# Kernel optimization log

Hardware: AMD Instinct MI355X
Metric: run time of the kernel (lower is better)

## Reference

```python
import jax, jax.numpy as jnp
import numpy as np

N = 50000          # nodes
E_RAND = 800000    # random edges (avg degree 16)
D_IN = 128
H = 4              # heads (both layers)
C = 64             # per-head channels (both layers)
NEG_SLOPE = 0.2    # PyG GATConv default leaky_relu slope


def _gat_conv(x, src, dst, W, att_src, att_dst, bias, concat):
    """PyG GATConv (dropout=0, self-loops already in edge list).
    x:[N,Din] W:[Din,H*C] att_*:[H,C] bias:[H*C] or [C]."""
    n = x.shape[0]
    h = (x @ W).reshape(n, H, C)                      # [N,H,C]
    a_src = jnp.sum(h * att_src, axis=-1)             # [N,H]
    a_dst = jnp.sum(h * att_dst, axis=-1)             # [N,H]
    e = jax.nn.leaky_relu(a_src[src] + a_dst[dst], NEG_SLOPE)  # [E,H]
    # segment softmax over incoming edges of each destination node
    m = jax.ops.segment_max(e, dst, num_segments=n)    # [N,H]
    e = jnp.exp(e - m[dst])
    denom = jax.ops.segment_sum(e, dst, num_segments=n)
    alpha = e / (denom[dst] + 1e-16)                   # [E,H]
    msg = h[src] * alpha[..., None]                    # [E,H,C]
    out = jax.ops.segment_sum(msg, dst, num_segments=n)  # [N,H,C]
    if concat:
        out = out.reshape(n, H * C)
    else:
        out = out.mean(axis=1)
    return out + bias


def setup_inputs() -> dict:
    key = jax.random.key(0)
    ks = jax.random.split(key, 10)
    x = jax.random.normal(ks[0], (N, D_IN), jnp.float32)
    src = jax.random.randint(ks[1], (E_RAND,), 0, N)
    dst = jax.random.randint(ks[2], (E_RAND,), 0, N)
    loops = jnp.arange(N)  # add_self_loops=True (PyG default)
    edge_index = jnp.stack([jnp.concatenate([src, loops]),
                            jnp.concatenate([dst, loops])]).astype(jnp.int32)
    g = lambda k, shp, fan: (jax.random.normal(k, shp, jnp.float32) / np.float32(np.sqrt(fan)))
    W1 = g(ks[3], (D_IN, H * C), D_IN)
    att_src1 = g(ks[4], (H, C), C)
    att_dst1 = g(ks[5], (H, C), C)
    b1 = jnp.zeros((H * C,), jnp.float32)
    W2 = g(ks[6], (H * C, H * C), H * C)
    att_src2 = g(ks[7], (H, C), C)
    att_dst2 = g(ks[8], (H, C), C)
    b2 = jnp.zeros((C,), jnp.float32)
    return {"x": x, "edge_index": edge_index,
            "W1": W1, "att_src1": att_src1, "att_dst1": att_dst1, "b1": b1,
            "W2": W2, "att_src2": att_src2, "att_dst2": att_dst2, "b2": b2}


def reference(x, edge_index, W1, att_src1, att_dst1, b1, W2, att_src2, att_dst2, b2):
    src, dst = edge_index[0], edge_index[1]
    h = jax.nn.relu(_gat_conv(x, src, dst, W1, att_src1, att_dst1, b1, concat=True))
    h = jax.nn.relu(_gat_conv(h, src, dst, W2, att_src2, att_dst2, b2, concat=False))
    return jax.nn.softmax(h, axis=1)
```

## Files before the change

kernel.cpp:

```cpp
#include <hip/hip_runtime.h>


typedef __attribute__((ext_vector_type(8))) short short8;
typedef __attribute__((ext_vector_type(4))) float f32x4;
typedef __attribute__((ext_vector_type(2))) float f32x2;

static __device__ __forceinline__ ushort f2bf(float f) {
  uint u = __float_as_uint(f);
  return (ushort)((u + 0x7FFFu + ((u >> 16) & 1u)) >> 16);
}
static __device__ __forceinline__ float bf2f(ushort s) {
  return __uint_as_float(((uint)s) << 16);
}
static __device__ __forceinline__ unsigned char f2fp8(float f) {
  int p = __builtin_amdgcn_cvt_pk_fp8_f32(f, f, 0, false);
  return (unsigned char)(p & 0xFF);
}
static __device__ __forceinline__ uint4 cvt8bf(const float4& a, const float4& b) {
  uint4 hh;
  hh.x = (uint)f2bf(a.x) | ((uint)f2bf(a.y) << 16);
  hh.y = (uint)f2bf(a.z) | ((uint)f2bf(a.w) << 16);
  hh.z = (uint)f2bf(b.x) | ((uint)f2bf(b.y) << 16);
  hh.w = (uint)f2bf(b.z) | ((uint)f2bf(b.w) << 16);
  return hh;
}

__global__ __launch_bounds__(256)
void k_prep_hist(const float* __restrict__ W1, const float* __restrict__ W2,
                 ushort* __restrict__ w1th, ushort* __restrict__ w1tl,
                 ushort* __restrict__ w2th, ushort* __restrict__ w2tl,
                 const int* __restrict__ dstv, int* __restrict__ cnt,
                 int* __restrict__ pe, int E,
                 const float* __restrict__ x, ushort* __restrict__ xb,
                 int ng ) {
  const int b = blockIdx.x;
  const int eb = (E + 255) >> 8;
  if (b < 128) {
    int gid = b * 256 + threadIdx.x;
    int c = gid & 255, k = gid >> 8;
    float w = W1[(size_t)k * 256 + c];
    ushort h = f2bf(w);
    w1th[(size_t)c * 128 + k] = h;
    w1tl[(size_t)c * 128 + k] = f2bf(w - bf2f(h));
  } else if (b < 384) {
    int gid = (b - 128) * 256 + threadIdx.x;
    int c = gid & 255, k = gid >> 8;
    float w = W2[(size_t)k * 256 + c];
    ushort h = f2bf(w);
    w2th[(size_t)c * 256 + k] = h;
    w2tl[(size_t)c * 256 + k] = f2bf(w - bf2f(h));
  } else if (b < 384 + eb) {
    int i = (b - 384) * 256 + threadIdx.x;
    if (i < E) pe[i] = atomicAdd(&cnt[dstv[i]], 1);
  } else {
    int i = (b - 384 - eb) * 256 + threadIdx.x;
    if (i < ng) {
      const float4* xp = (const float4*)x + (size_t)i * 2;
      float4 a = xp[0], bb = xp[1];
      ((uint4*)xb)[i] = cvt8bf(a, bb);
    }
  }
}

__global__ __launch_bounds__(256)
void k_scan(const int* __restrict__ cnt, int* __restrict__ rowptr,
            int* __restrict__ bsum, int* __restrict__ bflag, int N, int E) {
  __shared__ int sm[256];
  __shared__ int s_prev;
  const int b = blockIdx.x, tid = threadIdx.x;
  const int gid = b * 256 + tid;
  int v = (gid < N) ? cnt[gid] : 0;
  sm[tid] = v;
  __syncthreads();
  for (int off = 1; off < 256; off <<= 1) {
    int t = (tid >= off) ? sm[tid - off] : 0;
    __syncthreads();
    sm[tid] += t;
    __syncthreads();
  }
  if (tid == 255) {
    atomicExch(&bsum[b], sm[255]);
    __threadfence();
    atomicExch(&bflag[b], 1);
  }
  if (tid == 0) s_prev = 0;
  __syncthreads();
  if (tid < b) {
    while (atomicAdd(&bflag[tid], 0) == 0) {}
    atomicAdd(&s_prev, atomicAdd(&bsum[tid], 0));
  }
  __syncthreads();
  if (gid < N) rowptr[gid] = s_prev + sm[tid] - v;
  if (gid == 0) rowptr[N] = E;
}

template <int K>
static __device__ __forceinline__
void gemm_body(int bid, const ushort* __restrict__ Ah,
               const ushort* __restrict__ Bth, const ushort* __restrict__ Btl,
               unsigned char* __restrict__ hout, int Nrows,
               const float* __restrict__ att_s, const float* __restrict__ att_d,
               float* __restrict__ a_s, float* __restrict__ a_d) {
  const int nrb = (Nrows + 127) >> 7;
  const int rb = (bid >> 4) * 8 + (bid & 7);
  const int ch = (bid >> 3) & 1;
  if (rb >= nrb) return;
  const int row0 = rb * 128;
  const int col0 = ch * 128;

  const int t = threadIdx.x;
  const int lane = t & 63;
  const int w = t >> 6;
  const int wr = (w >> 1) * 64;
  const int wc = (w & 1) * 64;

  const int fr = lane & 15;
  const int fq = lane >> 4;

  const ushort* arow[4];
#pragma unroll
  for (int r = 0; r < 4; r++) {
    int gr = row0 + wr + r * 16 + fr;
    gr = gr < Nrows ? gr : Nrows - 1;
    arow[r] = Ah + (size_t)gr * K + fq * 8;
  }
  const ushort* bb_h = Bth + (size_t)(col0 + wc + fr) * K + fq * 8;
  const ushort* bb_l = Btl + (size_t)(col0 + wc + fr) * K + fq * 8;

  f32x4 acc[4][4] = {};

#pragma unroll
  for (int k0 = 0; k0 < K; k0 += 32) {
    short8 fa[4], fbh[4], fbl[4];
#pragma unroll
    for (int r = 0; r < 4; r++)
      fa[r] = *(const short8*)(arow[r] + k0);
#pragma unroll
    for (int c = 0; c < 4; c++) {
      fbh[c] = *(const short8*)(bb_h + (size_t)c * 16 * K + k0);
      fbl[c] = *(const short8*)(bb_l + (size_t)c * 16 * K + k0);
    }
#pragma unroll
    for (int r = 0; r < 4; r++)
#pragma unroll
      for (int c = 0; c < 4; c++) {
        acc[r][c] = __builtin_amdgcn_mfma_f32_16x16x32_bf16(fa[r], fbh[c], acc[r][c], 0, 0, 0);
        acc[r][c] = __builtin_amdgcn_mfma_f32_16x16x32_bf16(fa[r], fbl[c], acc[r][c], 0, 0, 0);
      }
  }

#pragma unroll
  for (int r = 0; r < 4; r++)
#pragma unroll
    for (int c = 0; c < 4; c++) {
      int colg = col0 + wc + c * 16 + fr;
#pragma unroll
      for (int reg = 0; reg < 4; reg++) {
        int gr = row0 + wr + r * 16 + fq * 4 + reg;
        if (gr < Nrows)
          hout[(size_t)gr * 256 + colg] = f2fp8(acc[r][c][reg]);
      }
    }

  const int head = (col0 + wc) >> 6;
  float asv[4], adv[4];
#pragma unroll
  for (int c = 0; c < 4; c++) {
    asv[c] = att_s[col0 + wc + c * 16 + fr];
    adv[c] = att_d[col0 + wc + c * 16 + fr];
  }
#pragma unroll
  for (int r = 0; r < 4; r++)
#pragma unroll
    for (int reg = 0; reg < 4; reg++) {
      float ps = 0.f, pd = 0.f;
#pragma unroll
      for (int c = 0; c < 4; c++) {
        ps += acc[r][c][reg] * asv[c];
        pd += acc[r][c][reg] * adv[c];
      }
      ps += __shfl_xor(ps, 1); pd += __shfl_xor(pd, 1);
      ps += __shfl_xor(ps, 2); pd += __shfl_xor(pd, 2);
      ps += __shfl_xor(ps, 4); pd += __shfl_xor(pd, 4);
      ps += __shfl_xor(ps, 8); pd += __shfl_xor(pd, 8);
      if (fr == 0) {
        int gr = row0 + wr + r * 16 + fq * 4 + reg;
        if (gr < Nrows) {
          a_s[(size_t)gr * 4 + head] = ps;
          a_d[(size_t)gr * 4 + head] = pd;
        }
      }
    }
}

__global__ __launch_bounds__(256, 2)
void k_gemm1_scatter(const ushort* __restrict__ xb,
                     const ushort* __restrict__ Bth,
                     const ushort* __restrict__ Btl,
                     unsigned char* __restrict__ hout, int Nrows,
                     const float* __restrict__ att_s,
                     const float* __restrict__ att_d,
                     float* __restrict__ a_s, float* __restrict__ a_d,
                     const int* __restrict__ srcv, const int* __restrict__ dstv,
                     const int* __restrict__ rowptr, const int* __restrict__ pe,
                     int* __restrict__ col, int E, int gemm_blocks) {
  if ((int)blockIdx.x < gemm_blocks) {
    gemm_body<128>(blockIdx.x, xb, Bth, Btl, hout, Nrows,
                   att_s, att_d, a_s, a_d);
  } else {
    int base = ((int)blockIdx.x - gemm_blocks) * 1024 + threadIdx.x;
#pragma unroll
    for (int k = 0; k < 4; k++) {
      int i = base + k * 256;
      if (i < E) col[rowptr[dstv[i]] + pe[i]] = srcv[i];
    }
  }
}

__global__ __launch_bounds__(256, 2)
void k_gemm2(const ushort* __restrict__ Ah,
             const ushort* __restrict__ Bth, const ushort* __restrict__ Btl,
             unsigned char* __restrict__ hout, int Nrows,
             const float* __restrict__ att_s, const float* __restrict__ att_d,
             float* __restrict__ a_s, float* __restrict__ a_d) {
  gemm_body<256>(blockIdx.x, Ah, Bth, Btl, hout, Nrows,
                 att_s, att_d, a_s, a_d);
}

template <int LAYER>
__global__ __launch_bounds__(256)
void k_aggr(const unsigned char* __restrict__ hsrc,
            const int* __restrict__ rowptr, const int* __restrict__ col,
            const float* __restrict__ a_s, const float* __restrict__ a_d,
            const float* __restrict__ bias,
            ushort* __restrict__ out_h, float* __restrict__ outp, int N) {
  __shared__ int   s_sh[4][64];
  __shared__ float w_sh[4][256];
  const int wv = threadIdx.x >> 6;
  const int lane = threadIdx.x & 63;
  const int node = blockIdx.x * 4 + wv;
  if (node >= N) return;
  const int hd = lane >> 4;
  const int beg = rowptr[node], end = rowptr[node + 1];
  const float4 adst = *(const float4*)(a_d + (size_t)node * 4);

  float4 acc = make_float4(0.f, 0.f, 0.f, 0.f);
  float wsum = 0.f;
  const char* hbase = (const char*)hsrc + lane * 4;

  for (int c0 = beg; c0 < end; c0 += 64) {
    int nc = min(64, end - c0);
    int s = 0;
    float4 w4 = make_float4(0.f, 0.f, 0.f, 0.f);
    if (lane < nc) {
      s = col[c0 + lane];
      float4 a = *(const float4*)(a_s + (size_t)s * 4);
      float e0 = a.x + adst.x; e0 = e0 > 0.f ? e0 : 0.2f * e0;
      float e1 = a.y + adst.y; e1 = e1 > 0.f ? e1 : 0.2f * e1;
      float e2 = a.z + adst.z; e2 = e2 > 0.f ? e2 : 0.2f * e2;
      float e3 = a.w + adst.w; e3 = e3 > 0.f ? e3 : 0.2f * e3;
      w4 = make_float4(__expf(e0), __expf(e1), __expf(e2), __expf(e3));
    }
    s_sh[wv][lane] = s;
    *(float4*)(&w_sh[wv][lane * 4]) = w4;
    asm volatile("s_waitcnt lgkmcnt(0)" ::: "memory");

    const float* wrow = &w_sh[wv][hd];
    const int*   srow = &s_sh[wv][0];
    int j = 0;
    for (; j + 4 <= nc; j += 4) {
      int sj0 = srow[j], sj1 = srow[j + 1], sj2 = srow[j + 2], sj3 = srow[j + 3];
      float w0 = wrow[4 * j],      w1 = wrow[4 * j + 4];
      float w2 = wrow[4 * j + 8],  w3 = wrow[4 * j + 12];
      uint p0 = *(const uint*)(hbase + ((size_t)((uint)sj0 << 8)));
      uint p1 = *(const uint*)(hbase + ((size_t)((uint)sj1 << 8)));
      uint p2 = *(const uint*)(hbase + ((size_t)((uint)sj2 << 8)));
      uint p3 = *(const uint*)(hbase + ((size_t)((uint)sj3 << 8)));
      f32x2 l0 = __builtin_amdgcn_cvt_pk_f32_fp8(p0, false);
      f32x2 h0 = __builtin_amdgcn_cvt_pk_f32_fp8(p0, true);
      f32x2 l1 = __builtin_amdgcn_cvt_pk_f32_fp8(p1, false);
      f32x2 h1 = __builtin_amdgcn_cvt_pk_f32_fp8(p1, true);
      f32x2 l2 = __builtin_amdgcn_cvt_pk_f32_fp8(p2, false);
      f32x2 h2 = __builtin_amdgcn_cvt_pk_f32_fp8(p2, true);
      f32x2 l3 = __builtin_amdgcn_cvt_pk_f32_fp8(p3, false);
      f32x2 h3 = __builtin_amdgcn_cvt_pk_f32_fp8(p3, true);
      wsum += w0 + w1 + w2 + w3;
      acc.x += w0 * l0.x; acc.y += w0 * l0.y; acc.z += w0 * h0.x; acc.w += w0 * h0.y;
      acc.x += w1 * l1.x; acc.y += w1 * l1.y; acc.z += w1 * h1.x; acc.w += w1 * h1.y;
      acc.x += w2 * l2.x; acc.y += w2 * l2.y; acc.z += w2 * h2.x; acc.w += w2 * h2.y;
      acc.x += w3 * l3.x; acc.y += w3 * l3.y; acc.z += w3 * h3.x; acc.w += w3 * h3.y;
    }
    for (; j < nc; j++) {
      int sj = srow[j];
      float ww = wrow[4 * j];
      uint p = *(const uint*)(hbase + ((size_t)((uint)sj << 8)));
      f32x2 lo = __builtin_amdgcn_cvt_pk_f32_fp8(p, false);
      f32x2 hi = __builtin_amdgcn_cvt_pk_f32_fp8(p, true);
      wsum += ww;
      acc.x += ww * lo.x; acc.y += ww * lo.y;
      acc.z += ww * hi.x; acc.w += ww * hi.y;
    }
  }

  float inv = 1.0f / wsum;
  float4 v = make_float4(acc.x * inv, acc.y * inv, acc.z * inv, acc.w * inv);

  if (LAYER == 1) {
    const float4 bv = *(const float4*)(bias + lane * 4);
    v.x = fmaxf(v.x + bv.x, 0.f);
    v.y = fmaxf(v.y + bv.y, 0.f);
    v.z = fmaxf(v.z + bv.z, 0.f);
    v.w = fmaxf(v.w + bv.w, 0.f);
    ushort4 h;
    h.x = f2bf(v.x); h.y = f2bf(v.y); h.z = f2bf(v.z); h.w = f2bf(v.w);
    *(ushort4*)(out_h + (size_t)node * 256 + lane * 4) = h;
  } else {
    v.x += __shfl_xor(v.x, 16); v.y += __shfl_xor(v.y, 16);
    v.z += __shfl_xor(v.z, 16); v.w += __shfl_xor(v.w, 16);
    v.x += __shfl_xor(v.x, 32); v.y += __shfl_xor(v.y, 32);
    v.z += __shfl_xor(v.z, 32); v.w += __shfl_xor(v.w, 32);
    const int c4 = (lane & 15) * 4;
    const float4 bv = *(const float4*)(bias + c4);
    v.x = fmaxf(v.x * 0.25f + bv.x, 0.f);
    v.y = fmaxf(v.y * 0.25f + bv.y, 0.f);
    v.z = fmaxf(v.z * 0.25f + bv.z, 0.f);
    v.w = fmaxf(v.w * 0.25f + bv.w, 0.f);
    float mx = fmaxf(fmaxf(v.x, v.y), fmaxf(v.z, v.w));
    for (int off = 8; off >= 1; off >>= 1) mx = fmaxf(mx, __shfl_xor(mx, off));
    v.x = __expf(v.x - mx); v.y = __expf(v.y - mx);
    v.z = __expf(v.z - mx); v.w = __expf(v.w - mx);
    float sum = v.x + v.y + v.z + v.w;
    for (int off = 8; off >= 1; off >>= 1) sum += __shfl_xor(sum, off);
    float is = 1.0f / sum;
    v.x *= is; v.y *= is; v.z *= is; v.w *= is;
    if (lane < 16) *(float4*)(outp + (size_t)node * 64 + c4) = v;
  }
}


extern "C" void kernel_launch(void* const* d_in, const int* in_sizes, int n_in,
                              void* d_out, int out_size, void* d_ws, size_t ws_size,
                              hipStream_t stream) {
  const float* x   = (const float*)d_in[0];
  const int*   ei  = (const int*)d_in[1];
  const float* W1  = (const float*)d_in[2];
  const float* as1 = (const float*)d_in[3];
  const float* ad1 = (const float*)d_in[4];
  const float* b1  = (const float*)d_in[5];
  const float* W2  = (const float*)d_in[6];
  const float* as2 = (const float*)d_in[7];
  const float* ad2 = (const float*)d_in[8];
  const float* b2  = (const float*)d_in[9];
  float* out = (float*)d_out;

  const int N = in_sizes[0] / 128;
  const int E = in_sizes[1] / 2;
  const int* srcv = ei;
  const int* dstv = ei + E;

  unsigned char* h8 = (unsigned char*)d_ws;
  ushort* hb   = (ushort*)(h8 + (size_t)N * 256);
  ushort* w1th = hb + (size_t)N * 256;
  ushort* w1tl = w1th + 256 * 128;
  ushort* w2th = w1tl + 256 * 128;
  ushort* w2tl = w2th + 256 * 256;
  float*  zbuf = (float*)(w2tl + 256 * 256);
  float* a_s1 = zbuf;
  float* a_d1 = a_s1 + (size_t)N * 4;
  float* a_s2 = a_d1 + (size_t)N * 4;
  float* a_d2 = a_s2 + (size_t)N * 4;
  int* rowptr = (int*)(zbuf + (size_t)N * 16);
  int* cnt    = rowptr + (N + 4);
  int* bflag  = cnt + N;
  int* bsum   = bflag + 256;
  int* pe     = bsum + 256;
  int* colx   = pe + E;
  ushort* xb  = (ushort*)(colx + E);

  const int nb = (N + 255) / 256;
  const int eb = (E + 255) / 256;
  const int eb4 = (E + 1023) / 1024;
  const int ng = N * 16;
  const int xcb = (ng + 255) / 256;

  const int nrb = (N + 127) / 128;
  const int gemm_blocks = ((nrb + 7) / 8) * 16;
  const int wb = (N + 3) / 4;

  hipMemsetAsync(cnt, 0, ((size_t)N + 256) * 4, stream);
  k_prep_hist<<<384 + eb + xcb, 256, 0, stream>>>(
      W1, W2, w1th, w1tl, w2th, w2tl, dstv, cnt, pe, E, x, xb, ng);
  k_scan<<<nb, 256, 0, stream>>>(cnt, rowptr, bsum, bflag, N, E);
  k_gemm1_scatter<<<gemm_blocks + eb4, 256, 0, stream>>>(
      xb, w1th, w1tl, h8, N, as1, ad1, a_s1, a_d1,
      srcv, dstv, rowptr, pe, colx, E, gemm_blocks);
  k_aggr<1><<<wb, 256, 0, stream>>>(h8, rowptr, colx, a_s1, a_d1, b1,
                                    hb, nullptr, N);
  k_gemm2<<<gemm_blocks, 256, 0, stream>>>(hb, w2th, w2tl, h8, N,
                                           as2, ad2, a_s2, a_d2);
  k_aggr<2><<<wb, 256, 0, stream>>>(h8, rowptr, colx, a_s2, a_d2, b2,
                                    nullptr, out, N);
}
```

Measured before the change: 308.3 us.

## Stage GEMM operand tiles through double-buffered LDS via direct global-to-LDS loads

Rewrites the shared GEMM body so A and the split-bf16 B tiles are copied into double-buffered LDS with global_load_lds, overlapping the next k-slice fetch with MFMA on the current one. Fragments are then read from LDS, replacing the strided direct-from-global loads each wave issued before. It also relaxes the launch bounds occupancy hint on both GEMM kernels. The cost is a barrier per k-step, 48KB of LDS per block, and possible LDS bank conflicts from the unpadded 32-wide rows.

```diff
diff --git a/kernel.cpp b/kernel.cpp
--- a/kernel.cpp
+++ b/kernel.cpp
@@ -23,6 +23,11 @@
   hh.z = (uint)f2bf(b.x) | ((uint)f2bf(b.y) << 16);
   hh.w = (uint)f2bf(b.z) | ((uint)f2bf(b.w) << 16);
   return hh;
+}
+static __device__ __forceinline__ void gl16(const ushort* g, ushort* l) {
+  __builtin_amdgcn_global_load_lds(
+      (const __attribute__((address_space(1))) uint*)(g),
+      (__attribute__((address_space(3))) uint*)(l), 16, 0, 0);
 }
 
 __global__ __launch_bounds__(256)
@@ -101,6 +106,10 @@
                unsigned char* __restrict__ hout, int Nrows,
                const float* __restrict__ att_s, const float* __restrict__ att_d,
                float* __restrict__ a_s, float* __restrict__ a_d) {
+  __shared__ ushort Asb[2][128][32];
+  __shared__ ushort Bhb[2][128][32];
+  __shared__ ushort Blb[2][128][32];
+
   const int nrb = (Nrows + 127) >> 7;
   const int rb = (bid >> 4) * 8 + (bid & 7);
   const int ch = (bid >> 3) & 1;
@@ -113,32 +122,49 @@
   const int w = t >> 6;
   const int wr = (w >> 1) * 64;
   const int wc = (w & 1) * 64;
-
   const int fr = lane & 15;
   const int fq = lane >> 4;
 
-  const ushort* arow[4];
-#pragma unroll
-  for (int r = 0; r < 4; r++) {
-    int gr = row0 + wr + r * 16 + fr;
-    gr = gr < Nrows ? gr : Nrows - 1;
-    arow[r] = Ah + (size_t)gr * K + fq * 8;
-  }
-  const ushort* bb_h = Bth + (size_t)(col0 + wc + fr) * K + fq * 8;
-  const ushort* bb_l = Btl + (size_t)(col0 + wc + fr) * K + fq * 8;
+  const int srow = lane >> 2;
+  const int skc = (lane & 3) * 8;
+  int ar0 = row0 + w * 32 + srow;
+  int ar1 = ar0 + 16;
+  ar0 = ar0 < Nrows ? ar0 : Nrows - 1;
+  ar1 = ar1 < Nrows ? ar1 : Nrows - 1;
+  const ushort* agp0 = Ah + (size_t)ar0 * K + skc;
+  const ushort* agp1 = Ah + (size_t)ar1 * K + skc;
+  const ushort* bhg0 = Bth + (size_t)(col0 + w * 32 + srow) * K + skc;
+  const ushort* bhg1 = bhg0 + (size_t)16 * K;
+  const ushort* blg0 = Btl + (size_t)(col0 + w * 32 + srow) * K + skc;
+  const ushort* blg1 = blg0 + (size_t)16 * K;
 
   f32x4 acc[4][4] = {};
 
-#pragma unroll
-  for (int k0 = 0; k0 < K; k0 += 32) {
+  auto stage = [&](int buf, int k0) {
+    gl16(agp0 + k0, &Asb[buf][w * 32][0]);
+    gl16(agp1 + k0, &Asb[buf][w * 32 + 16][0]);
+    gl16(bhg0 + k0, &Bhb[buf][w * 32][0]);
+    gl16(bhg1 + k0, &Bhb[buf][w * 32 + 16][0]);
+    gl16(blg0 + k0, &Blb[buf][w * 32][0]);
+    gl16(blg1 + k0, &Blb[buf][w * 32 + 16][0]);
+  };
+
+  stage(0, 0);
+  const int NK = K / 32;
+#pragma unroll
+  for (int ks = 0; ks < NK; ks++) {
+    const int buf = ks & 1;
+    __syncthreads();
+    if (ks + 1 < NK) stage(buf ^ 1, (ks + 1) * 32);
+
     short8 fa[4], fbh[4], fbl[4];
 #pragma unroll
     for (int r = 0; r < 4; r++)
-      fa[r] = *(const short8*)(arow[r] + k0);
+      fa[r] = *(const short8*)(&Asb[buf][wr + r * 16 + fr][fq * 8]);
 #pragma unroll
     for (int c = 0; c < 4; c++) {
-      fbh[c] = *(const short8*)(bb_h + (size_t)c * 16 * K + k0);
-      fbl[c] = *(const short8*)(bb_l + (size_t)c * 16 * K + k0);
+      fbh[c] = *(const short8*)(&Bhb[buf][wc + c * 16 + fr][fq * 8]);
+      fbl[c] = *(const short8*)(&Blb[buf][wc + c * 16 + fr][fq * 8]);
     }
 #pragma unroll
     for (int r = 0; r < 4; r++)
@@ -193,7 +219,7 @@
     }
 }
 
-__global__ __launch_bounds__(256, 2)
+__global__ __launch_bounds__(256)
 void k_gemm1_scatter(const ushort* __restrict__ xb,
                      const ushort* __restrict__ Bth,
                      const ushort* __restrict__ Btl,
@@ -217,7 +243,7 @@
   }
 }
 
-__global__ __launch_bounds__(256, 2)
+__global__ __launch_bounds__(256)
 void k_gemm2(const ushort* __restrict__ Ah,
              const ushort* __restrict__ Bth, const ushort* __restrict__ Btl,
              unsigned char* __restrict__ hout, int Nrows,
```

New measurement: 275.7 us. -10.6%, faster.
